# Performance work log

Measured on AMD Instinct MI355X. Metric: run time of the kernel, lower is better.

Reference implementation:

```python
import jax, jax.numpy as jnp
import numpy as np

B, H, W, C = 32, 256, 256, 3
KH, KW, F = 5, 5, 8


def setup_inputs() -> dict:
    key = jax.random.key(0)
    k1, k2 = jax.random.split(key)
    x = jax.random.normal(k1, (B, H, W, C), dtype=jnp.float32)
    # learned structuring elements, shape (KH, KW, C, F) per build()
    kernel = jax.random.normal(k2, (KH, KW, C, F), dtype=jnp.float32) * 0.1
    return {"x": x, "kernel": kernel}


def _max_of_erosions(x, kernel):
    # tf.nn.erosion2d semantics: out[b,y,x,c] = min_{dy,dx} in[b, y+dy-pt, x+dx-pl, c]
    #                                               - kernel[KH-1-dy, KW-1-dx, c]
    # (erosion = -dilation(-x, reversed kernel)); then channel-max per filter.
    Bq, Hq, Wq, Cq = x.shape
    kh, kw, _, nf = kernel.shape
    pad_h, pad_w = kh - 1, kw - 1          # stride 1, rate 1, SAME padding
    pt, pl = pad_h // 2, pad_w // 2
    xp = jnp.pad(x, ((0, 0), (pt, pad_h - pt), (pl, pad_w - pl), (0, 0)),
                 constant_values=jnp.inf)   # +inf is identity for min
    kflip = kernel[::-1, ::-1]              # reflected structuring element
    ero = None                              # running min over window taps
    for dy in range(kh):                    # small fixed 5x5 tap loop
        for dx in range(kw):
            win = xp[:, dy:dy + Hq, dx:dx + Wq, :]          # [B,H,W,C]
            cand = win[..., None] - kflip[dy, dx]           # [B,H,W,C,F]
            ero = cand if ero is None else jnp.minimum(ero, cand)
    return jnp.max(ero, axis=3)             # channel max -> [B,H,W,F]


def reference(x, kernel):
    return _max_of_erosions(x, kernel)
```

## Files before the change

### kernel.cpp

```cpp
#include <hip/hip_runtime.h>
#include <math.h>


#define Hq 256

__global__ __launch_bounds__(256) void maxero_sg(
    const float* __restrict__ x,
    const float* __restrict__ kern,
    float* __restrict__ out)
{
    __shared__ float xt[3][5][264];

    const int tid = threadIdx.x;
    const int bI  = blockIdx.x;
    const int b   = bI >> 8;
    const int h   = bI & 255;

    const float INF = __builtin_inff();
    const float* xb = x + (size_t)b * (Hq * 256 * 3);

    #pragma unroll
    for (int r = 0; r < 5; ++r) {
        int rr  = h - 2 + r;
        bool rv = (unsigned)rr < 256u;
        int rc  = min(max(rr, 0), 255);
        const float* p = xb + rc * 768 + tid * 3;
        float v0 = p[0], v1 = p[1], v2 = p[2];
        xt[0][r][tid + 2] = rv ? v0 : INF;
        xt[1][r][tid + 2] = rv ? v1 : INF;
        xt[2][r][tid + 2] = rv ? v2 : INF;
    }
    if (tid < 60) {
        int cr = tid >> 2;
        int c  = cr / 5, r = cr - 5 * c;
        int q  = tid & 3;
        int idx = (q < 2) ? q : 256 + q;
        xt[c][r][idx] = INF;
    }
    __syncthreads();

    float acc[3][8];
    #pragma unroll
    for (int c = 0; c < 3; ++c)
        #pragma unroll
        for (int f = 0; f < 8; ++f)
            acc[c][f] = INF;

    #pragma unroll
    for (int dy = 0; dy < 5; ++dy) {
        float xr[3][5];
        #pragma unroll
        for (int c = 0; c < 3; ++c)
            #pragma unroll
            for (int j = 0; j < 5; ++j)
                xr[c][j] = xt[c][dy][tid + j];

        #pragma unroll
        for (int c = 0; c < 3; ++c) {
            #pragma unroll
            for (int f = 0; f < 8; ++f) {
                float k0 = kern[((4 - dy) * 5 + 4) * 24 + c * 8 + f];
                float k1 = kern[((4 - dy) * 5 + 3) * 24 + c * 8 + f];
                float k2 = kern[((4 - dy) * 5 + 2) * 24 + c * 8 + f];
                float k3 = kern[((4 - dy) * 5 + 1) * 24 + c * 8 + f];
                float k4 = kern[((4 - dy) * 5 + 0) * 24 + c * 8 + f];
                float a  = acc[c][f];
                a = fminf(fminf(a, xr[c][0] - k0), xr[c][1] - k1);
                a = fminf(fminf(a, xr[c][2] - k2), xr[c][3] - k3);
                acc[c][f] = fminf(a, xr[c][4] - k4);
            }
        }
    }

    float4 oA, oB;
    oA.x = fmaxf(fmaxf(acc[0][0], acc[1][0]), acc[2][0]);
    oA.y = fmaxf(fmaxf(acc[0][1], acc[1][1]), acc[2][1]);
    oA.z = fmaxf(fmaxf(acc[0][2], acc[1][2]), acc[2][2]);
    oA.w = fmaxf(fmaxf(acc[0][3], acc[1][3]), acc[2][3]);
    oB.x = fmaxf(fmaxf(acc[0][4], acc[1][4]), acc[2][4]);
    oB.y = fmaxf(fmaxf(acc[0][5], acc[1][5]), acc[2][5]);
    oB.z = fmaxf(fmaxf(acc[0][6], acc[1][6]), acc[2][6]);
    oB.w = fmaxf(fmaxf(acc[0][7], acc[1][7]), acc[2][7]);

    float* op = out + ((size_t)b * 65536 + (size_t)h * 256 + tid) * 8;
    reinterpret_cast<float4*>(op)[0] = oA;
    reinterpret_cast<float4*>(op)[1] = oB;
}

extern "C" void kernel_launch(void* const* d_in, const int* in_sizes, int n_in,
                              void* d_out, int out_size, void* d_ws, size_t ws_size,
                              hipStream_t stream) {
    const float* x    = (const float*)d_in[0];
    const float* kern = (const float*)d_in[1];
    float* out        = (float*)d_out;
    maxero_sg<<<8192, 256, 0, stream>>>(x, kern, out);
}
```

Baseline: 52.39 us.

## Tile 4x128 pixels per block, assign one filter per wavefront, use min3/max3

Each block now covers a 4-row by 128-column tile, so the 2-row halo is loaded once for four output rows instead of once per row. Each wavefront handles a single filter, which makes its kernel weights wave-uniform scalar loads. Each lane computes 8 consecutive pixels from a 36-value window read with float4 LDS loads. The min/max reductions use v_min3/v_max3 inline assembly, and the output is transposed through LDS so the final stores are coalesced. In exchange the tiling is more complex and the kernel needs extra LDS traffic and barriers for the transpose.

```diff
diff --git a/kernel.cpp b/kernel.cpp
--- a/kernel.cpp
+++ b/kernel.cpp
@@ -2,89 +2,124 @@
 #include <math.h>
 
 
-#define Hq 256
+#define INFF __builtin_inff()
 
-__global__ __launch_bounds__(256) void maxero_sg(
+static __device__ __forceinline__ float min3f(float a, float b, float c) {
+    float d;
+    asm("v_min3_f32 %0, %1, %2, %3" : "=v"(d) : "v"(a), "v"(b), "v"(c));
+    return d;
+}
+static __device__ __forceinline__ float max3f(float a, float b, float c) {
+    float d;
+    asm("v_max3_f32 %0, %1, %2, %3" : "=v"(d) : "v"(a), "v"(b), "v"(c));
+    return d;
+}
+
+__global__ __launch_bounds__(512) void maxero_fw(
     const float* __restrict__ x,
     const float* __restrict__ kern,
     float* __restrict__ out)
 {
-    __shared__ float xt[3][5][264];
+    __shared__ __align__(16) float smem[4192];
 
     const int tid = threadIdx.x;
     const int bI  = blockIdx.x;
-    const int b   = bI >> 8;
-    const int h   = bI & 255;
+    const int b   = bI >> 7;
+    const int rem = bI & 127;
+    const int h0  = (rem >> 1) << 2;
+    const int c0  = (rem & 1) << 7;
 
-    const float INF = __builtin_inff();
-    const float* xb = x + (size_t)b * (Hq * 256 * 3);
+    const float* xb = x + (size_t)b * (256 * 256 * 3);
 
     #pragma unroll
-    for (int r = 0; r < 5; ++r) {
-        int rr  = h - 2 + r;
-        bool rv = (unsigned)rr < 256u;
-        int rc  = min(max(rr, 0), 255);
-        const float* p = xb + rc * 768 + tid * 3;
-        float v0 = p[0], v1 = p[1], v2 = p[2];
-        xt[0][r][tid + 2] = rv ? v0 : INF;
-        xt[1][r][tid + 2] = rv ? v1 : INF;
-        xt[2][r][tid + 2] = rv ? v2 : INF;
+    for (int k2 = 0; k2 < 2; ++k2) {
+        int ch = tid + k2 * 512;
+        if (ch < 768) {
+            int rr = ch / 96;
+            int e  = ch - rr * 96;
+            int gr = h0 - 2 + rr;
+            bool rv = (unsigned)gr < 256u;
+            int rc = min(max(gr, 0), 255);
+            float4 v = *(const float4*)(xb + rc * 768 + c0 * 3 + e * 4);
+            float* d = &smem[rr * 408 + 6 + e * 4];
+            ((float2*)d)[0] = rv ? make_float2(v.x, v.y) : make_float2(INFF, INFF);
+            ((float2*)d)[1] = rv ? make_float2(v.z, v.w) : make_float2(INFF, INFF);
+        }
     }
-    if (tid < 60) {
-        int cr = tid >> 2;
-        int c  = cr / 5, r = cr - 5 * c;
-        int q  = tid & 3;
-        int idx = (q < 2) ? q : 256 + q;
-        xt[c][r][idx] = INF;
+    if (tid < 96) {
+        int rr = tid / 12, q = tid - rr * 12;
+        int cs = q / 3, c = q - cs * 3;
+        int lcol = (cs < 2) ? cs : 128 + cs;
+        int gc   = (cs < 2) ? (c0 - 2 + cs) : (c0 + 126 + cs);
+        int gr   = h0 - 2 + rr;
+        bool v = ((unsigned)gr < 256u) && ((unsigned)gc < 256u);
+        int rc = min(max(gr, 0), 255), cc = min(max(gc, 0), 255);
+        smem[rr * 408 + lcol * 3 + c] = v ? xb[rc * 768 + cc * 3 + c] : INFF;
     }
     __syncthreads();
 
-    float acc[3][8];
+    const int lane = tid & 63;
+    const int f    = __builtin_amdgcn_readfirstlane(tid >> 6);
+    const int r    = lane >> 4;
+    const int g    = lane & 15;
+
+    float acc[8][3];
     #pragma unroll
-    for (int c = 0; c < 3; ++c)
-        #pragma unroll
-        for (int f = 0; f < 8; ++f)
-            acc[c][f] = INF;
+    for (int p = 0; p < 8; ++p) { acc[p][0] = INFF; acc[p][1] = INFF; acc[p][2] = INFF; }
 
     #pragma unroll
     for (int dy = 0; dy < 5; ++dy) {
-        float xr[3][5];
+        float xr[36];
+        const float4* wp = (const float4*)&smem[(r + dy) * 408 + g * 24];
+        #pragma unroll
+        for (int q4 = 0; q4 < 9; ++q4) {
+            float4 t = wp[q4];
+            xr[q4*4+0] = t.x; xr[q4*4+1] = t.y; xr[q4*4+2] = t.z; xr[q4*4+3] = t.w;
+        }
+        float sk[15];
+        #pragma unroll
+        for (int dx = 0; dx < 5; ++dx)
+            #pragma unroll
+            for (int c = 0; c < 3; ++c)
+                sk[dx * 3 + c] = kern[((4 - dy) * 5 + (4 - dx)) * 24 + c * 8 + f];
         #pragma unroll
         for (int c = 0; c < 3; ++c)
             #pragma unroll
-            for (int j = 0; j < 5; ++j)
-                xr[c][j] = xt[c][dy][tid + j];
-
-        #pragma unroll
-        for (int c = 0; c < 3; ++c) {
-            #pragma unroll
-            for (int f = 0; f < 8; ++f) {
-                float k0 = kern[((4 - dy) * 5 + 4) * 24 + c * 8 + f];
-                float k1 = kern[((4 - dy) * 5 + 3) * 24 + c * 8 + f];
-                float k2 = kern[((4 - dy) * 5 + 2) * 24 + c * 8 + f];
-                float k3 = kern[((4 - dy) * 5 + 1) * 24 + c * 8 + f];
-                float k4 = kern[((4 - dy) * 5 + 0) * 24 + c * 8 + f];
-                float a  = acc[c][f];
-                a = fminf(fminf(a, xr[c][0] - k0), xr[c][1] - k1);
-                a = fminf(fminf(a, xr[c][2] - k2), xr[c][3] - k3);
-                acc[c][f] = fminf(a, xr[c][4] - k4);
+            for (int p = 0; p < 8; ++p) {
+                float d0 = xr[(p + 0) * 3 + c] - sk[0 * 3 + c];
+                float d1 = xr[(p + 1) * 3 + c] - sk[1 * 3 + c];
+                float d2 = xr[(p + 2) * 3 + c] - sk[2 * 3 + c];
+                float d3 = xr[(p + 3) * 3 + c] - sk[3 * 3 + c];
+                float d4 = xr[(p + 4) * 3 + c] - sk[4 * 3 + c];
+                float a = min3f(acc[p][c], d0, d1);
+                a = min3f(a, d2, d3);
+                acc[p][c] = fminf(a, d4);
             }
-        }
     }
 
-    float4 oA, oB;
-    oA.x = fmaxf(fmaxf(acc[0][0], acc[1][0]), acc[2][0]);
-    oA.y = fmaxf(fmaxf(acc[0][1], acc[1][1]), acc[2][1]);
-    oA.z = fmaxf(fmaxf(acc[0][2], acc[1][2]), acc[2][2]);
-    oA.w = fmaxf(fmaxf(acc[0][3], acc[1][3]), acc[2][3]);
-    oB.x = fmaxf(fmaxf(acc[0][4], acc[1][4]), acc[2][4]);
-    oB.y = fmaxf(fmaxf(acc[0][5], acc[1][5]), acc[2][5]);
-    oB.z = fmaxf(fmaxf(acc[0][6], acc[1][6]), acc[2][6]);
-    oB.w = fmaxf(fmaxf(acc[0][7], acc[1][7]), acc[2][7]);
+    float o[8];
+    #pragma unroll
+    for (int p = 0; p < 8; ++p) o[p] = max3f(acc[p][0], acc[p][1], acc[p][2]);
 
-    float* op = out + ((size_t)b * 65536 + (size_t)h * 256 + tid) * 8;
-    reinterpret_cast<float4*>(op)[0] = oA;
-    reinterpret_cast<float4*>(op)[1] = oB;
+    __syncthreads();
+    {
+        float* ol = smem;
+        int px0 = r * 128 + 8 * g;
+        ((float4*)&ol[f * 524 + px0])[0] = make_float4(o[0], o[1], o[2], o[3]);
+        ((float4*)&ol[f * 524 + px0])[1] = make_float4(o[4], o[5], o[6], o[7]);
+    }
+    __syncthreads();
+    {
+        float v0 = smem[0 * 524 + tid], v1 = smem[1 * 524 + tid];
+        float v2 = smem[2 * 524 + tid], v3 = smem[3 * 524 + tid];
+        float v4 = smem[4 * 524 + tid], v5 = smem[5 * 524 + tid];
+        float v6 = smem[6 * 524 + tid], v7 = smem[7 * 524 + tid];
+        float* op = out + ((size_t)b * 65536
+                           + (size_t)(h0 + (tid >> 7)) * 256
+                           + c0 + (tid & 127)) * 8;
+        ((float4*)op)[0] = make_float4(v0, v1, v2, v3);
+        ((float4*)op)[1] = make_float4(v4, v5, v6, v7);
+    }
 }
 
 extern "C" void kernel_launch(void* const* d_in, const int* in_sizes, int n_in,
@@ -93,5 +128,5 @@
     const float* x    = (const float*)d_in[0];
     const float* kern = (const float*)d_in[1];
     float* out        = (float*)d_out;
-    maxero_sg<<<8192, 256, 0, stream>>>(x, kern, out);
+    maxero_fw<<<4096, 512, 0, stream>>>(x, kern, out);
 }
```

New measurement: 59.47 us. 13.5% more time.
